# Performance work log

Hardware: AMD Instinct MI355X
Metric: run time of the kernel (lower is better)

The kernel has to match this reference:

```python
import jax, jax.numpy as jnp
import numpy as np

TEMPERATURE = 0.5  # module buffer `temperature`


def setup_inputs() -> dict:
    key = jax.random.key(0)
    emb_in = jax.random.normal(key, (8192, 1024), dtype=jnp.float32)
    return {"emb_in": emb_in}


def reference(emb_in):
    B = emb_in.shape[0]
    n = B // 4  # loop bound in the original module
    # F.normalize(emb_in, dim=1); after normalization cosine_similarity == dot product
    z = emb_in / jnp.linalg.norm(emb_in, axis=1, keepdims=True)
    S = jnp.matmul(z, z.T) / jnp.float32(TEMPERATURE)  # [B, B] sim / temperature
    rows = S[:n]  # only rows i < n are ever used               # [n, B]
    idx = jnp.arange(n)
    exp_rows = jnp.exp(rows)
    # denominator_i = sum_{k != i} exp(sim[i,k]/T) over the FULL batch dimension
    denom = exp_rows.sum(axis=1) - exp_rows[idx, idx]           # [n]
    log_denom = jnp.log(denom)
    # loss_ij = -(S[i,j] - log(denom_i)); summed over i < j < n.
    # For each i there are (n-1-i) values of j, each contributing log_denom[i].
    counts = (n - 1) - idx                                      # [n]
    sum_sim = jnp.sum(jnp.triu(rows[:, :n], k=1))               # sum_{i<j} S[i,j]/T
    loss = jnp.sum(counts.astype(log_denom.dtype) * log_denom) - sum_sim
    return (-2.0 / n) * (n - 1) * loss
```

## Files before the change

### kernel.cpp

```cpp
#include <hip/hip_runtime.h>
#include <stdint.h>


#define BDIM 1024
#define BROWS 8192
#define NROWS 2048

#define BM 256
#define BN 256
#define BKB 128
#define NKT (BDIM / BKB)

typedef __attribute__((ext_vector_type(4))) int i32x4;
typedef __attribute__((ext_vector_type(8))) int i32x8;
typedef __attribute__((ext_vector_type(4))) float f32x4;

static __device__ __forceinline__ unsigned char f2e4m3(float x) {
  uint32_t u = __float_as_uint(x);
  uint32_t s = (u >> 24) & 0x80u;
  uint32_t a = u & 0x7fffffffu;
  if (a == 0) return (unsigned char)s;
  int e = (int)(a >> 23) - 127;
  uint32_t m = a & 0x7fffffu;
  if (e >= -6) {
    uint32_t keep = m >> 20;
    uint32_t rest = m & 0xfffffu;
    keep += (rest > 0x80000u) || (rest == 0x80000u && (keep & 1u));
    uint32_t v = ((uint32_t)(e + 7) << 3) + keep;
    return (unsigned char)(s | v);
  }
  if (e < -10) return (unsigned char)s;
  uint32_t full = 0x800000u | m;
  int sh = 14 - e;
  uint32_t keep = full >> sh;
  uint32_t rest = full & ((1u << sh) - 1u);
  uint32_t half = 1u << (sh - 1);
  keep += (rest > half) || (rest == half && (keep & 1u));
  return (unsigned char)(s | keep);
}

static __device__ __forceinline__ void gload_lds16(const unsigned char* g, unsigned char* l) {
  __builtin_amdgcn_global_load_lds(
      (const __attribute__((address_space(1))) uint32_t*)(const void*)g,
      (__attribute__((address_space(3))) uint32_t*)(void*)l,
      16, 0, 0);
}

static __device__ __forceinline__ uint32_t pk4(float4 v, float inv) {
  return (uint32_t)f2e4m3(v.x * inv) | ((uint32_t)f2e4m3(v.y * inv) << 8) |
         ((uint32_t)f2e4m3(v.z * inv) << 16) | ((uint32_t)f2e4m3(v.w * inv) << 24);
}

__global__ __launch_bounds__(256) void normalize_kernel(const float* __restrict__ emb,
                                                        unsigned char* __restrict__ zb,
                                                        float* __restrict__ denom,
                                                        float* __restrict__ sumsim) {
  const int w = threadIdx.x >> 6;
  const int lane = threadIdx.x & 63;
  const int row = blockIdx.x * 4 + w;
  const float4* src = reinterpret_cast<const float4*>(emb + (size_t)row * BDIM);
  float4 v[4];
  float ss = 0.f;
#pragma unroll
  for (int i = 0; i < 4; i++) {
    v[i] = src[lane * 4 + i];
    ss += v[i].x * v[i].x + v[i].y * v[i].y + v[i].z * v[i].z + v[i].w * v[i].w;
  }
#pragma unroll
  for (int m = 1; m < 64; m <<= 1) ss += __shfl_xor(ss, m);
  const float inv = rsqrtf(ss);
  uint4 o;
  o.x = pk4(v[0], inv);
  o.y = pk4(v[1], inv);
  o.z = pk4(v[2], inv);
  o.w = pk4(v[3], inv);
  const int cp = (lane & 56) | ((lane & 7) ^ (row & 7));
  *reinterpret_cast<uint4*>(zb + (size_t)row * BDIM + cp * 16) = o;
  if (blockIdx.x < NROWS / 4 && lane == 0) denom[row] = 0.f;
  if (blockIdx.x == 0 && threadIdx.x == 0) sumsim[0] = 0.f;
}


__global__ __launch_bounds__(1024) void gemm_fused(const unsigned char* __restrict__ zb,
                                                   float* __restrict__ denom,
                                                   float* __restrict__ sumsim) {
  __shared__ unsigned char As[2][BM * BKB];
  __shared__ unsigned char Bs[2][BN * BKB];

  const int bx = blockIdx.x;
  const int xcd = bx & 7;
  const int idx = bx >> 3;
  const int jb = xcd * 4 + (idx & 3);
  const int ib = idx >> 2;
  const int i0 = ib * BM;
  const int j0 = jb * BN;

  const int t = threadIdx.x;
  const int lane = t & 63;
  const int w = t >> 6;
  const int WR = w >> 2;
  const int WC = w & 3;

  const int rsh = lane >> 3;
  const int lin = (lane & 7) * 16;
  const int aw = w * 16;

  const int q2 = lane >> 4;
  const int rsub = lane & 15;
  const int rk = rsub & 7;

  f32x4 acc[4][4] = {};

#define STG_A(buf, r0, kk) \
  gload_lds16(zb + (size_t)(i0 + (r0) + aw + rsh) * BDIM + (kk) + lin, &As[buf][((r0) + aw) * BKB])
#define STG_B(buf, r0, kk) \
  gload_lds16(zb + (size_t)(j0 + (r0) + aw + rsh) * BDIM + (kk) + lin, &Bs[buf][((r0) + aw) * BKB])

#define RD_FRAG(dst, base, row)                                                                                  \
  {                                                                                                              \
    const i32x4 lo = *reinterpret_cast<const i32x4*>(&base[(size_t)(row) * BKB + (((2 * q2) ^ rk) * 16)]);       \
    const i32x4 hi = *reinterpret_cast<const i32x4*>(&base[(size_t)(row) * BKB + (((2 * q2 + 1) ^ rk) * 16)]);   \
    dst[0] = lo[0]; dst[1] = lo[1]; dst[2] = lo[2]; dst[3] = lo[3];                                              \
    dst[4] = hi[0]; dst[5] = hi[1]; dst[6] = hi[2]; dst[7] = hi[3];                                              \
  }

#define STAGE_TILE(buf, kk)                        \
  {                                                \
    STG_A(buf, 0, kk); STG_A(buf, 8, kk);          \
    STG_B(buf, 0, kk); STG_B(buf, 8, kk);          \
  }

  STAGE_TILE(0, 0);
  __syncthreads();

  int cur = 0;
#pragma unroll 1
  for (int kt = 0; kt < NKT; ++kt) {
    const int nb = cur ^ 1;
    if (kt + 1 < NKT) STAGE_TILE(nb, (kt + 1) * BKB);

    i32x8 bb[4];
#pragma unroll
    for (int nn = 0; nn < 4; nn++) {
      RD_FRAG(bb[nn], (&Bs[cur][0]), WC * 64 + nn * 16 + rsub);
    }
    __builtin_amdgcn_s_setprio(1);
#pragma unroll
    for (int mm = 0; mm < 4; mm++) {
      i32x8 aa;
      RD_FRAG(aa, (&As[cur][0]), WR * 64 + mm * 16 + rsub);
#pragma unroll
      for (int nn = 0; nn < 4; nn++) {
        acc[mm][nn] = __builtin_amdgcn_mfma_scale_f32_16x16x128_f8f6f4(
            aa, bb[nn], acc[mm][nn], 0, 0, 0, 0x7f7f7f7f, 0, 0x7f7f7f7f);
      }
    }
    __builtin_amdgcn_s_setprio(0);

    __syncthreads();
    cur = nb;
  }

  const int hi4 = lane >> 4;
  const int col_l = lane & 15;
  float ssim = 0.f;
#pragma unroll
  for (int m = 0; m < 4; m++) {
    const int gibase = i0 + WR * 64 + m * 16 + hi4 * 4;
#pragma unroll
    for (int r = 0; r < 4; r++) {
      const int gi = gibase + r;
      float dsum = 0.f;
#pragma unroll
      for (int n = 0; n < 4; n++) {
        const int gj = j0 + WC * 64 + n * 16 + col_l;
        const float s = acc[m][n][r] * 2.0f;
        const float e = __expf(s);
        if (gj != gi) dsum += e;
        if (gj < NROWS && gi < gj) ssim += s;
      }
      dsum += __shfl_xor(dsum, 1);
      dsum += __shfl_xor(dsum, 2);
      dsum += __shfl_xor(dsum, 4);
      dsum += __shfl_xor(dsum, 8);
      if (col_l == 0) atomicAdd(&denom[gi], dsum);
    }
  }
#pragma unroll
  for (int msk = 1; msk < 64; msk <<= 1) ssim += __shfl_xor(ssim, msk);
  if (lane == 0 && j0 < NROWS) atomicAdd(sumsim, ssim);
}

__global__ __launch_bounds__(1024) void finalize(const float* __restrict__ denom,
                                                 const float* __restrict__ sumsim,
                                                 float* __restrict__ out) {
  const int t = threadIdx.x;
  double s = 0.0;
#pragma unroll
  for (int i = t; i < NROWS; i += 1024) {
    s += (double)(NROWS - 1 - i) * log((double)denom[i]);
  }
#pragma unroll
  for (int m = 1; m < 64; m <<= 1) s += __shfl_xor(s, m);
  __shared__ double ws_[16];
  if ((t & 63) == 0) ws_[t >> 6] = s;
  __syncthreads();
  if (t == 0) {
    double tot = 0.0;
#pragma unroll
    for (int i = 0; i < 16; i++) tot += ws_[i];
    const double loss = tot - (double)sumsim[0];
    out[0] = (float)(-2.0 / (double)NROWS * (double)(NROWS - 1) * loss);
  }
}

extern "C" void kernel_launch(void* const* d_in, const int* in_sizes, int n_in,
                              void* d_out, int out_size, void* d_ws, size_t ws_size,
                              hipStream_t stream) {
  const float* emb = (const float*)d_in[0];
  unsigned char* zb = (unsigned char*)d_ws;
  float* denom = (float*)((char*)d_ws + (size_t)BROWS * BDIM);
  float* sumsim = denom + NROWS;
  float* out = (float*)d_out;

  normalize_kernel<<<BROWS / 4, 256, 0, stream>>>(emb, zb, denom, sumsim);
  gemm_fused<<<(NROWS / BM) * (BROWS / BN), 1024, 0, stream>>>(zb, denom, sumsim);
  finalize<<<1, 1024, 0, stream>>>(denom, sumsim, out);
}
```

Before: 55.08 us.

## Shrink GEMM tile to 128x256 with single-buffered LDS and more resident blocks

```diff
diff --git a/kernel.cpp b/kernel.cpp
--- a/kernel.cpp
+++ b/kernel.cpp
@@ -6,7 +6,7 @@
 #define BROWS 8192
 #define NROWS 2048
 
-#define BM 256
+#define BM 128
 #define BN 256
 #define BKB 128
 #define NKT (BDIM / BKB)
@@ -81,11 +81,11 @@
 }
 
 
-__global__ __launch_bounds__(1024) void gemm_fused(const unsigned char* __restrict__ zb,
-                                                   float* __restrict__ denom,
-                                                   float* __restrict__ sumsim) {
-  __shared__ unsigned char As[2][BM * BKB];
-  __shared__ unsigned char Bs[2][BN * BKB];
+__global__ __launch_bounds__(512, 4) void gemm_fused(const unsigned char* __restrict__ zb,
+                                                     float* __restrict__ denom,
+                                                     float* __restrict__ sumsim) {
+  __shared__ unsigned char As[BM * BKB];
+  __shared__ unsigned char Bs[BN * BKB];
 
   const int bx = blockIdx.x;
   const int xcd = bx & 7;
@@ -103,7 +103,6 @@
 
   const int rsh = lane >> 3;
   const int lin = (lane & 7) * 16;
-  const int aw = w * 16;
 
   const int q2 = lane >> 4;
   const int rsub = lane & 15;
@@ -111,10 +110,10 @@
 
   f32x4 acc[4][4] = {};
 
-#define STG_A(buf, r0, kk) \
-  gload_lds16(zb + (size_t)(i0 + (r0) + aw + rsh) * BDIM + (kk) + lin, &As[buf][((r0) + aw) * BKB])
-#define STG_B(buf, r0, kk) \
-  gload_lds16(zb + (size_t)(j0 + (r0) + aw + rsh) * BDIM + (kk) + lin, &Bs[buf][((r0) + aw) * BKB])
+#define STG_A(g, kk) \
+  gload_lds16(zb + (size_t)(i0 + (g) * 8 + rsh) * BDIM + (kk) + lin, &As[(g) * 8 * BKB])
+#define STG_B(g, kk) \
+  gload_lds16(zb + (size_t)(j0 + (g) * 8 + rsh) * BDIM + (kk) + lin, &Bs[(g) * 8 * BKB])
 
 #define RD_FRAG(dst, base, row)                                                                                  \
   {                                                                                                              \
@@ -124,31 +123,24 @@
     dst[4] = hi[0]; dst[5] = hi[1]; dst[6] = hi[2]; dst[7] = hi[3];                                              \
   }
 
-#define STAGE_TILE(buf, kk)                        \
-  {                                                \
-    STG_A(buf, 0, kk); STG_A(buf, 8, kk);          \
-    STG_B(buf, 0, kk); STG_B(buf, 8, kk);          \
-  }
-
-  STAGE_TILE(0, 0);
-  __syncthreads();
-
-  int cur = 0;
 #pragma unroll 1
   for (int kt = 0; kt < NKT; ++kt) {
-    const int nb = cur ^ 1;
-    if (kt + 1 < NKT) STAGE_TILE(nb, (kt + 1) * BKB);
+    const int kk = kt * BKB;
+    STG_A(2 * w, kk); STG_A(2 * w + 1, kk);
+    STG_B(4 * w, kk); STG_B(4 * w + 1, kk);
+    STG_B(4 * w + 2, kk); STG_B(4 * w + 3, kk);
+    __syncthreads();
 
     i32x8 bb[4];
 #pragma unroll
     for (int nn = 0; nn < 4; nn++) {
-      RD_FRAG(bb[nn], (&Bs[cur][0]), WC * 64 + nn * 16 + rsub);
+      RD_FRAG(bb[nn], Bs, WC * 64 + nn * 16 + rsub);
     }
     __builtin_amdgcn_s_setprio(1);
 #pragma unroll
     for (int mm = 0; mm < 4; mm++) {
       i32x8 aa;
-      RD_FRAG(aa, (&As[cur][0]), WR * 64 + mm * 16 + rsub);
+      RD_FRAG(aa, As, WR * 64 + mm * 16 + rsub);
 #pragma unroll
       for (int nn = 0; nn < 4; nn++) {
         acc[mm][nn] = __builtin_amdgcn_mfma_scale_f32_16x16x128_f8f6f4(
@@ -156,9 +148,7 @@
       }
     }
     __builtin_amdgcn_s_setprio(0);
-
     __syncthreads();
-    cur = nb;
   }
 
   const int hi4 = lane >> 4;
@@ -224,6 +214,6 @@
   float* out = (float*)d_out;
 
   normalize_kernel<<<BROWS / 4, 256, 0, stream>>>(emb, zb, denom, sumsim);
-  gemm_fused<<<(NROWS / BM) * (BROWS / BN), 1024, 0, stream>>>(zb, denom, sumsim);
+  gemm_fused<<<(NROWS / BM) * (BROWS / BN), 512, 0, stream>>>(zb, denom, sumsim);
   finalize<<<1, 1024, 0, stream>>>(denom, sumsim, out);
 }
```

Result: slower. 59.02 us (+7.1%).
